# Performance work log

Measured on AMD Instinct MI355X. Metric: run time of the kernel, lower is better.

The kernel has to match this reference:

```python
import jax, jax.numpy as jnp
import numpy as np

B, N, C = 4, 20480, 128
H, HD = 8, 16           # num_heads, head_dim (C // H)
L = 4                   # number of WindowBasedGraphAttentionBlocks
NW, WS = 320, 64        # num_windows, window_size (N // NW)
SCALE = HD ** -0.5
EPS = 1e-5


def layernorm(x, g, b):
    mu = jnp.mean(x, axis=-1, keepdims=True)
    var = jnp.mean(jnp.square(x - mu), axis=-1, keepdims=True)
    return (x - mu) * jax.lax.rsqrt(var + EPS) * g + b


def setup_inputs() -> dict:
    key = jax.random.key(0)
    ks = jax.random.split(key, 8)
    x = jax.random.normal(ks[0], (B, N, C), dtype=jnp.float32)
    # geodesic window mapping: each of NW windows has exactly WS members, permuted
    window_ids = jnp.asarray(
        np.random.RandomState(0).permutation(np.repeat(np.arange(NW), WS)),
        dtype=jnp.int32)
    s = 0.02
    inp = {
        'x': x,
        'g1': jnp.ones((L, C), jnp.float32),
        'be1': jnp.zeros((L, C), jnp.float32),
        'Wqkv': jax.random.normal(ks[1], (L, C, 3 * C), jnp.float32) * s,
        'bqkv': jnp.zeros((L, 3 * C), jnp.float32),
        'rel_bias': jax.random.normal(ks[2], (L, H, 1, 1), jnp.float32) * s,
        'Wproj': jax.random.normal(ks[3], (L, C, C), jnp.float32) * s,
        'bproj': jnp.zeros((L, C), jnp.float32),
        'g2': jnp.ones((L, C), jnp.float32),
        'be2': jnp.zeros((L, C), jnp.float32),
        'W1': jax.random.normal(ks[4], (L, C, 4 * C), jnp.float32) * s,
        'b1': jnp.zeros((L, 4 * C), jnp.float32),
        'W2': jax.random.normal(ks[5], (L, 4 * C, C), jnp.float32) * s,
        'b2': jnp.zeros((L, C), jnp.float32),
        'window_ids': window_ids,
    }
    return inp


def _encoder(x, g1, be1, Wqkv, bqkv, rel_bias, Wproj, bproj, g2, be2,
             W1, b1, W2, b2, sort_idx, inv_idx):
    def step(x, p):
        (g1, be1, Wqkv, bqkv, rb, Wp, bp, g2, be2, W1, b1, W2, b2) = p
        shortcut = x
        # GeodesicWindowPartition: gather by argsort(window_ids), split into windows
        win = x[:, sort_idx, :].reshape(B * NW, WS, C)
        h = layernorm(win, g1, be1)
        qkv = (h @ Wqkv + bqkv).reshape(B * NW, WS, 3, H, HD)
        q = qkv[:, :, 0].transpose(0, 2, 1, 3)  # [BW, H, WS, HD]
        k = qkv[:, :, 1].transpose(0, 2, 1, 3)
        v = qkv[:, :, 2].transpose(0, 2, 1, 3)
        attn = jnp.einsum('whqd,whkd->whqk', q, k) * SCALE
        attn = attn + rb[None]                  # relative geometry bias [H,1,1]
        attn = jax.nn.softmax(attn, axis=-1)
        out = jnp.einsum('whqk,whkd->whqd', attn, v)
        out = out.transpose(0, 2, 1, 3).reshape(B * NW, WS, C)
        out = out @ Wp + bp                     # AttentionOutputProjection
        rec = out.reshape(B, N, C)[:, inv_idx, :]  # partition.reverse
        x = shortcut + rec
        h2 = layernorm(x, g2, be2)
        x = x + (jax.nn.gelu(h2 @ W1 + b1) @ W2 + b2)
        return x, None

    params = (g1, be1, Wqkv, bqkv, rel_bias, Wproj, bproj, g2, be2, W1, b1, W2, b2)
    x, _ = jax.lax.scan(step, x, params)
    return x


def reference(x, g1, be1, Wqkv, bqkv, rel_bias, Wproj, bproj, g2, be2,
              W1, b1, W2, b2, window_ids):
    sort_idx = jnp.argsort(window_ids)
    inv_idx = jnp.argsort(sort_idx)
    return _encoder(x, g1, be1, Wqkv, bqkv, rel_bias, Wproj, bproj, g2, be2,
                    W1, b1, W2, b2, sort_idx, inv_idx)
```

## Files before the change

### kernel.cpp

```cpp
#include <hip/hip_runtime.h>
#include <hip/hip_bf16.h>
#include <math.h>

#define Nn 20480
#define Cc 128
#define Hh 8
#define Ll 4
#define NWw 320
#define BN 81920

typedef short sv8 __attribute__((ext_vector_type(8)));
typedef __bf16 bfv8 __attribute__((ext_vector_type(8)));
typedef float f32x4 __attribute__((ext_vector_type(4)));

__device__ __forceinline__ f32x4 mfma16(sv8 a, sv8 b, f32x4 c) {
    return __builtin_amdgcn_mfma_f32_16x16x32_bf16(
        __builtin_bit_cast(bfv8, a), __builtin_bit_cast(bfv8, b), c, 0, 0, 0);
}
__device__ __forceinline__ ushort f2bf(float f) {
    uint u = __float_as_uint(f);
    u += 0x7fffu + ((u >> 16) & 1u);
    return (ushort)(u >> 16);
}
__device__ __forceinline__ float fast_gelu(float x) {
    float z = 0.7978845608f * (x + 0.044715f * x * x * x);
    return x * __builtin_amdgcn_rcpf(1.0f + __expf(-2.0f * z));
}

__global__ __launch_bounds__(64) void rank_kernel(const int* __restrict__ wid,
        int* __restrict__ lrank, int* __restrict__ hist) {
    __shared__ int keys[64];
    int c = blockIdx.x, lane = threadIdx.x;
    for (int j = lane; j < NWw; j += 64) hist[c * NWw + j] = 0;
    int i = c * 64 + lane;
    int w = wid[i];
    keys[lane] = w;
    __syncthreads();
    int rank = 0, total = 0;
    for (int j = 0; j < 64; ++j) {
        int kj = keys[j];
        total += (kj == w);
        rank += (j < lane && kj == w) ? 1 : 0;
    }
    lrank[i] = rank;
    if (rank == 0) hist[c * NWw + w] = total;
}
__global__ __launch_bounds__(64) void prefix_kernel(int* __restrict__ hist) {
    int w = blockIdx.x, lane = threadIdx.x;
    int running = 0;
    for (int it = 0; it < NWw / 64; ++it) {
        int c = it * 64 + lane;
        int v = hist[c * NWw + w];
        int orig = v;
        #pragma unroll
        for (int d = 1; d < 64; d <<= 1) {
            int tt = __shfl_up(v, d, 64);
            if (lane >= d) v += tt;
        }
        hist[c * NWw + w] = running + v - orig;
        running += __shfl(v, 63, 64);
    }
}
__global__ __launch_bounds__(64) void scatter_kernel(const int* __restrict__ wid,
        const int* __restrict__ lrank, const int* __restrict__ hist,
        int* __restrict__ sidx) {
    int c = blockIdx.x, lane = threadIdx.x;
    int i = c * 64 + lane;
    int w = wid[i];
    sidx[w * 64 + hist[c * NWw + w] + lrank[i]] = i;
}

__global__ __launch_bounds__(256) void wconv_kernel(
    const float* __restrict__ Wqkv, const float* __restrict__ Wproj,
    const float* __restrict__ W1, const float* __restrict__ W2,
    ushort* __restrict__ wt) {
    int id = blockIdx.x * 256 + threadIdx.x;
    int l = id / 196608;
    int r = id % 196608;
    const float* src; int dst;
    if (r < 49152) { int n = r % 384, k = r / 384;
        src = Wqkv + l * 49152 + k * 384 + n; dst = l * 196608 + n * 128 + k; }
    else if (r < 65536) { int rr = r - 49152; int n = rr % 128, k = rr / 128;
        src = Wproj + l * 16384 + k * 128 + n; dst = l * 196608 + 49152 + n * 128 + k; }
    else if (r < 131072) { int rr = r - 65536; int n = rr % 512, k = rr / 512;
        src = W1 + l * 65536 + k * 512 + n; dst = l * 196608 + 65536 + n * 128 + k; }
    else { int rr = r - 131072; int n = rr % 128, k = rr / 128;
        src = W2 + l * 65536 + k * 128 + n; dst = l * 196608 + 131072 + n * 512 + k; }
    wt[dst] = f2bf(*src);
}

__global__ __launch_bounds__(256, 2) void attn_fused_kernel(
    const float* __restrict__ xsrc, float* __restrict__ xdst,
    const ushort* __restrict__ wqkvT, const float* __restrict__ bqkv,
    const float* __restrict__ relb, const ushort* __restrict__ wprojT,
    const float* __restrict__ bproj, const float* __restrict__ g1,
    const float* __restrict__ be1, const int* __restrict__ sidx) {
    __shared__ __align__(16) ushort hl_[64][128];
    __shared__ __align__(16) ushort qkn[64][256];
    __shared__ __align__(16) ushort vT[128][76];
    __shared__ __align__(16) ushort pt[4][16][76];
    __shared__ int ridx[64];

    int t = threadIdx.x;
    int wave = t >> 6, lane = t & 63;
    int lr = lane & 15, lg = lane >> 4;
    int wb = blockIdx.x;
    int bN = (wb / NWw) * Nn;
    int p0 = (wb % NWw) * 64;

    if (t < 64) ridx[t] = sidx[p0 + t];
    __syncthreads();

    {
        int hl2 = lane & 31, hb = lane >> 5;
        float4 gg = *(const float4*)(g1 + hl2 * 4);
        float4 bb = *(const float4*)(be1 + hl2 * 4);
        #pragma unroll
        for (int it = 0; it < 8; ++it) {
            int row = it * 8 + wave * 2 + hb;
            int gi = bN + ridx[row];
            float4 v = *(const float4*)(xsrc + (size_t)gi * Cc + hl2 * 4);
            float s = v.x + v.y + v.z + v.w;
            s += __shfl_xor(s, 1, 64);  s += __shfl_xor(s, 2, 64);
            s += __shfl_xor(s, 4, 64);  s += __shfl_xor(s, 8, 64);
            s += __shfl_xor(s, 16, 64);
            float mu = s * 0.0078125f;
            float d0 = v.x - mu, d1 = v.y - mu, d2 = v.z - mu, d3 = v.w - mu;
            float q = d0 * d0 + d1 * d1 + d2 * d2 + d3 * d3;
            q += __shfl_xor(q, 1, 64);  q += __shfl_xor(q, 2, 64);
            q += __shfl_xor(q, 4, 64);  q += __shfl_xor(q, 8, 64);
            q += __shfl_xor(q, 16, 64);
            float rs = rsqrtf(q * 0.0078125f + 1e-5f);
            uint2 pk;
            pk.x = (uint)f2bf(d0 * rs * gg.x + bb.x) | ((uint)f2bf(d1 * rs * gg.y + bb.y) << 16);
            pk.y = (uint)f2bf(d2 * rs * gg.z + bb.z) | ((uint)f2bf(d3 * rs * gg.w + bb.w) << 16);
            *(uint2*)&hl_[row][(hl2 * 4) ^ ((row & 7) << 3)] = pk;
        }
    }
    __syncthreads();

    {
        f32x4 acc[4][6] = {};
        #pragma unroll
        for (int ks = 0; ks < 4; ++ks) {
            int k0 = ks * 32 + lg * 8;
            sv8 a[4], b[6];
            #pragma unroll
            for (int rf = 0; rf < 4; ++rf) {
                int row = rf * 16 + lr;
                a[rf] = *(const sv8*)&hl_[row][k0 ^ ((row & 7) << 3)];
            }
            #pragma unroll
            for (int nf = 0; nf < 6; ++nf) {
                int gcol = (nf < 2 ? 32 * wave + nf * 16
                          : nf < 4 ? 128 + 32 * wave + (nf - 2) * 16
                                   : 256 + 32 * wave + (nf - 4) * 16) + lr;
                b[nf] = *(const sv8*)(wqkvT + (size_t)gcol * 128 + k0);
            }
            #pragma unroll
            for (int rf = 0; rf < 4; ++rf)
                #pragma unroll
                for (int nf = 0; nf < 6; ++nf)
                    acc[rf][nf] = mfma16(a[rf], b[nf], acc[rf][nf]);
        }
        #pragma unroll
        for (int nf = 0; nf < 6; ++nf) {
            int gcol = (nf < 2 ? 32 * wave + nf * 16
                      : nf < 4 ? 128 + 32 * wave + (nf - 2) * 16
                               : 256 + 32 * wave + (nf - 4) * 16) + lr;
            float bs = bqkv[gcol];
            if (nf < 4) {
                #pragma unroll
                for (int rf = 0; rf < 4; ++rf)
                    #pragma unroll
                    for (int r = 0; r < 4; ++r) {
                        int row = rf * 16 + lg * 4 + r;
                        qkn[row][gcol ^ ((row & 7) << 3)] = f2bf(acc[rf][nf][r] + bs);
                    }
            } else {
                int dcol = gcol - 256;
                #pragma unroll
                for (int rf = 0; rf < 4; ++rf) {
                    uint2 pk;
                    pk.x = (uint)f2bf(acc[rf][nf][0] + bs) | ((uint)f2bf(acc[rf][nf][1] + bs) << 16);
                    pk.y = (uint)f2bf(acc[rf][nf][2] + bs) | ((uint)f2bf(acc[rf][nf][3] + bs) << 16);
                    *(uint2*)&vT[dcol][rf * 16 + lg * 4] = pk;
                }
            }
        }
    }
    __syncthreads();

    f32x4 zz = {0.f, 0.f, 0.f, 0.f};
    #pragma unroll
    for (int hi = 0; hi < 2; ++hi) {
        int hh = wave * 2 + hi;
        float rb = relb[hh];
        sv8 bv[2];
        #pragma unroll
        for (int ks = 0; ks < 2; ++ks)
            bv[ks] = *(const sv8*)&vT[hh * 16 + lr][ks * 32 + lg * 8];
        sv8 aq[4], bk[4];
        sv8 z = {0, 0, 0, 0, 0, 0, 0, 0};
        bool lo = (lg < 2);
        #pragma unroll
        for (int f = 0; f < 4; ++f) {
            aq[f] = z; bk[f] = z;
            if (lo) {
                int row = f * 16 + lr;
                aq[f] = *(const sv8*)&qkn[row][(hh * 16 + lg * 8) ^ ((row & 7) << 3)];
                bk[f] = *(const sv8*)&qkn[row][(128 + hh * 16 + lg * 8) ^ ((row & 7) << 3)];
            }
        }
        f32x4 s[4][4];
        #pragma unroll
        for (int kt = 0; kt < 4; ++kt)
            #pragma unroll
            for (int qt = 0; qt < 4; ++qt)
                s[kt][qt] = mfma16(bk[kt], aq[qt], zz);

        f32x4 o[4];
        #pragma unroll
        for (int qt = 0; qt < 4; ++qt) {
            float v[16];
            #pragma unroll
            for (int kt = 0; kt < 4; ++kt)
                #pragma unroll
                for (int r = 0; r < 4; ++r)
                    v[kt * 4 + r] = s[kt][qt][r] * 0.25f + rb;
            float m0 = fmaxf(fmaxf(fmaxf(v[0], v[1]), fmaxf(v[2], v[3])),
                             fmaxf(fmaxf(v[4], v[5]), fmaxf(v[6], v[7])));
            float m1 = fmaxf(fmaxf(fmaxf(v[8], v[9]), fmaxf(v[10], v[11])),
                             fmaxf(fmaxf(v[12], v[13]), fmaxf(v[14], v[15])));
            float mx = fmaxf(m0, m1);
            mx = fmaxf(mx, __shfl_xor(mx, 16, 64));
            mx = fmaxf(mx, __shfl_xor(mx, 32, 64));
            float sum = 0.f;
            #pragma unroll
            for (int i = 0; i < 16; ++i) {
                v[i] = __expf(v[i] - mx);
                sum += v[i];
            }
            sum += __shfl_xor(sum, 16, 64);
            sum += __shfl_xor(sum, 32, 64);
            float inv = __builtin_amdgcn_rcpf(sum);
            #pragma unroll
            for (int kt = 0; kt < 4; ++kt) {
                uint2 pk;
                pk.x = (uint)f2bf(v[kt * 4 + 0] * inv) | ((uint)f2bf(v[kt * 4 + 1] * inv) << 16);
                pk.y = (uint)f2bf(v[kt * 4 + 2] * inv) | ((uint)f2bf(v[kt * 4 + 3] * inv) << 16);
                *(uint2*)&pt[wave][lr][kt * 16 + lg * 4] = pk;
            }
            sv8 ap0 = *(const sv8*)&pt[wave][lr][lg * 8];
            sv8 ap1 = *(const sv8*)&pt[wave][lr][32 + lg * 8];
            o[qt] = mfma16(ap0, bv[0], zz);
            o[qt] = mfma16(ap1, bv[1], o[qt]);
        }
        #pragma unroll
        for (int qt = 0; qt < 4; ++qt)
            #pragma unroll
            for (int r = 0; r < 4; ++r) {
                int row = qt * 16 + lg * 4 + r;
                hl_[row][(hh * 16 + lr) ^ ((row & 7) << 3)] = f2bf(o[qt][r]);
            }
    }
    __syncthreads();

    {
        f32x4 acc[4][2] = {};
        #pragma unroll
        for (int ks = 0; ks < 4; ++ks) {
            int k0 = ks * 32 + lg * 8;
            sv8 a[4], b[2];
            #pragma unroll
            for (int rf = 0; rf < 4; ++rf) {
                int row = rf * 16 + lr;
                a[rf] = *(const sv8*)&hl_[row][k0 ^ ((row & 7) << 3)];
            }
            #pragma unroll
            for (int nf = 0; nf < 2; ++nf)
                b[nf] = *(const sv8*)(wprojT + (size_t)(wave * 32 + nf * 16 + lr) * 128 + k0);
            #pragma unroll
            for (int rf = 0; rf < 4; ++rf)
                #pragma unroll
                for (int nf = 0; nf < 2; ++nf)
                    acc[rf][nf] = mfma16(a[rf], b[nf], acc[rf][nf]);
        }
        #pragma unroll
        for (int nf = 0; nf < 2; ++nf) {
            int col = wave * 32 + nf * 16 + lr;
            float bs = bproj[col];
            #pragma unroll
            for (int rf = 0; rf < 4; ++rf)
                #pragma unroll
                for (int r = 0; r < 4; ++r) {
                    int row = rf * 16 + lg * 4 + r;
                    int gi = bN + ridx[row];
                    size_t ad = (size_t)gi * Cc + col;
                    xdst[ad] = xsrc[ad] + acc[rf][nf][r] + bs;
                }
        }
    }
}

__global__ __launch_bounds__(256, 2) void mlp_fused_kernel(
    const float* __restrict__ xsrc, float* __restrict__ xdst,
    const ushort* __restrict__ w1T, const float* __restrict__ b1,
    const ushort* __restrict__ w2T, const float* __restrict__ b2,
    const float* __restrict__ g2, const float* __restrict__ be2) {
    __shared__ __align__(16) ushort hl_[64][128];
    __shared__ __align__(16) ushort hid[64][512];
    int t = threadIdx.x, wave = t >> 6, lane = t & 63;
    int lr = lane & 15, lg = lane >> 4;
    int r0 = blockIdx.x * 64;

    {
        int hl2 = lane & 31, hb = lane >> 5;
        float4 gg = *(const float4*)(g2 + hl2 * 4);
        float4 bb = *(const float4*)(be2 + hl2 * 4);
        #pragma unroll
        for (int it = 0; it < 8; ++it) {
            int row = it * 8 + wave * 2 + hb;
            float4 v = *(const float4*)(xsrc + (size_t)(r0 + row) * Cc + hl2 * 4);
            float s = v.x + v.y + v.z + v.w;
            s += __shfl_xor(s, 1, 64);  s += __shfl_xor(s, 2, 64);
            s += __shfl_xor(s, 4, 64);  s += __shfl_xor(s, 8, 64);
            s += __shfl_xor(s, 16, 64);
            float mu = s * 0.0078125f;
            float d0 = v.x - mu, d1 = v.y - mu, d2 = v.z - mu, d3 = v.w - mu;
            float q = d0 * d0 + d1 * d1 + d2 * d2 + d3 * d3;
            q += __shfl_xor(q, 1, 64);  q += __shfl_xor(q, 2, 64);
            q += __shfl_xor(q, 4, 64);  q += __shfl_xor(q, 8, 64);
            q += __shfl_xor(q, 16, 64);
            float rs = rsqrtf(q * 0.0078125f + 1e-5f);
            uint2 pk;
            pk.x = (uint)f2bf(d0 * rs * gg.x + bb.x) | ((uint)f2bf(d1 * rs * gg.y + bb.y) << 16);
            pk.y = (uint)f2bf(d2 * rs * gg.z + bb.z) | ((uint)f2bf(d3 * rs * gg.w + bb.w) << 16);
            *(uint2*)&hl_[row][(hl2 * 4) ^ ((row & 7) << 3)] = pk;
        }
    }
    __syncthreads();

    {
        f32x4 acc[4][8] = {};
        #pragma unroll
        for (int ks = 0; ks < 4; ++ks) {
            int k0 = ks * 32 + lg * 8;
            sv8 a[4], b[8];
            #pragma unroll
            for (int rf = 0; rf < 4; ++rf) {
                int row = rf * 16 + lr;
                a[rf] = *(const sv8*)&hl_[row][k0 ^ ((row & 7) << 3)];
            }
            #pragma unroll
            for (int nf = 0; nf < 8; ++nf)
                b[nf] = *(const sv8*)(w1T + (size_t)(wave * 128 + nf * 16 + lr) * 128 + k0);
            #pragma unroll
            for (int rf = 0; rf < 4; ++rf)
                #pragma unroll
                for (int nf = 0; nf < 8; ++nf)
                    acc[rf][nf] = mfma16(a[rf], b[nf], acc[rf][nf]);
        }
        #pragma unroll
        for (int nf = 0; nf < 8; ++nf) {
            int col = wave * 128 + nf * 16 + lr;
            float bs = b1[col];
            #pragma unroll
            for (int rf = 0; rf < 4; ++rf)
                #pragma unroll
                for (int r = 0; r < 4; ++r) {
                    int row = rf * 16 + lg * 4 + r;
                    hid[row][col ^ ((row & 7) << 3)] = f2bf(fast_gelu(acc[rf][nf][r] + bs));
                }
        }
    }
    __syncthreads();

    {
        f32x4 acc2[4][2] = {};
        #pragma unroll
        for (int ks = 0; ks < 16; ++ks) {
            int k0 = ks * 32 + lg * 8;
            sv8 a[4], b[2];
            #pragma unroll
            for (int rf = 0; rf < 4; ++rf) {
                int row = rf * 16 + lr;
                a[rf] = *(const sv8*)&hid[row][k0 ^ ((row & 7) << 3)];
            }
            #pragma unroll
            for (int nf = 0; nf < 2; ++nf)
                b[nf] = *(const sv8*)(w2T + (size_t)(wave * 32 + nf * 16 + lr) * 512 + k0);
            #pragma unroll
            for (int rf = 0; rf < 4; ++rf)
                #pragma unroll
                for (int nf = 0; nf < 2; ++nf)
                    acc2[rf][nf] = mfma16(a[rf], b[nf], acc2[rf][nf]);
        }
        __syncthreads();
        float* fh = (float*)hid;
        #pragma unroll
        for (int nf = 0; nf < 2; ++nf) {
            int col = wave * 32 + nf * 16 + lr;
            float bs = b2[col];
            #pragma unroll
            for (int rf = 0; rf < 4; ++rf)
                #pragma unroll
                for (int r = 0; r < 4; ++r) {
                    int row = rf * 16 + lg * 4 + r;
                    fh[row * 132 + col] = acc2[rf][nf][r] + bs;
                }
        }
        __syncthreads();
        #pragma unroll
        for (int j = 0; j < 8; ++j) {
            int idx = t + j * 256;
            int row = idx >> 5, c4 = (idx & 31) * 4;
            size_t ad = (size_t)(r0 + row) * Cc + c4;
            float4 xv = *(const float4*)(xsrc + ad);
            float4 hv = *(const float4*)&fh[row * 132 + c4];
            float4 ov = {xv.x + hv.x, xv.y + hv.y, xv.z + hv.z, xv.w + hv.w};
            *(float4*)(xdst + ad) = ov;
        }
    }
}

extern "C" void kernel_launch(void* const* d_in, const int* in_sizes, int n_in,
                              void* d_out, int out_size, void* d_ws, size_t ws_size,
                              hipStream_t stream) {
    const float* x_in   = (const float*)d_in[0];
    const float* g1     = (const float*)d_in[1];
    const float* be1    = (const float*)d_in[2];
    const float* Wqkv   = (const float*)d_in[3];
    const float* bqkv   = (const float*)d_in[4];
    const float* relb   = (const float*)d_in[5];
    const float* Wproj  = (const float*)d_in[6];
    const float* bproj  = (const float*)d_in[7];
    const float* g2     = (const float*)d_in[8];
    const float* be2    = (const float*)d_in[9];
    const float* W1     = (const float*)d_in[10];
    const float* b1     = (const float*)d_in[11];
    const float* W2     = (const float*)d_in[12];
    const float* b2     = (const float*)d_in[13];
    const int*   wid    = (const int*)d_in[14];

    size_t off = 0;
    float* x_ws = (float*)d_ws;                      off += (size_t)BN * Cc * 4;
    ushort* wt  = (ushort*)((char*)d_ws + off);      off += (size_t)786432 * 2;
    int* sidx   = (int*)((char*)d_ws + off);         off += (size_t)Nn * 4;
    int* lrank  = (int*)((char*)d_ws + off);         off += (size_t)Nn * 4;
    int* hist   = (int*)((char*)d_ws + off);         off += (size_t)NWw * NWw * 4;
    if (ws_size < off) return;

    rank_kernel<<<Nn / 64, 64, 0, stream>>>(wid, lrank, hist);
    prefix_kernel<<<NWw, 64, 0, stream>>>(hist);
    scatter_kernel<<<Nn / 64, 64, 0, stream>>>(wid, lrank, hist, sidx);
    wconv_kernel<<<786432 / 256, 256, 0, stream>>>(Wqkv, Wproj, W1, W2, wt);

    for (int l = 0; l < Ll; ++l) {
        const ushort* wqkvT  = wt + (size_t)l * 196608;
        const ushort* wprojT = wqkvT + 49152;
        const ushort* w1T    = wqkvT + 65536;
        const ushort* w2T    = wqkvT + 131072;
        const float* xsrc = (l == 0) ? x_in : x_ws;

        attn_fused_kernel<<<BN / 64, 256, 0, stream>>>(
            xsrc, x_ws, wqkvT, bqkv + l * 384, relb + l * Hh,
            wprojT, bproj + l * Cc, g1 + l * Cc, be1 + l * Cc, sidx);

        float* xdst = (l == Ll - 1) ? (float*)d_out : x_ws;
        mlp_fused_kernel<<<BN / 64, 256, 0, stream>>>(
            x_ws, xdst, w1T, b1 + l * 512, w2T, b2 + l * Cc,
            g2 + l * Cc, be2 + l * Cc);
    }
}
```

Measured before the change: 471.8 us.

## Chunk MLP hidden dimension with double-buffered LDS and use packed bf16 conversion

The MLP kernel now processes the 512-wide hidden layer in four 128-column chunks, holding only two chunk buffers in LDS (48KB total instead of 80KB). This cuts the accumulator register footprint, which allows a launch bound of three blocks per CU instead of two. The cost is an extra barrier per chunk. Separately, the software round-to-nearest bf16 packing is replaced by the hardware v_cvt_pk_bf16_f32 instruction in the layernorm, V-transpose and softmax stores.

```diff
diff --git a/kernel.cpp b/kernel.cpp
--- a/kernel.cpp
+++ b/kernel.cpp
@@ -21,6 +21,11 @@
     uint u = __float_as_uint(f);
     u += 0x7fffu + ((u >> 16) & 1u);
     return (ushort)(u >> 16);
+}
+__device__ __forceinline__ uint pk2bf(float lo, float hi) {
+    uint r;
+    asm("v_cvt_pk_bf16_f32 %0, %1, %2" : "=v"(r) : "v"(lo), "v"(hi));
+    return r;
 }
 __device__ __forceinline__ float fast_gelu(float x) {
     float z = 0.7978845608f * (x + 0.044715f * x * x * x);
@@ -132,8 +137,8 @@
             q += __shfl_xor(q, 16, 64);
             float rs = rsqrtf(q * 0.0078125f + 1e-5f);
             uint2 pk;
-            pk.x = (uint)f2bf(d0 * rs * gg.x + bb.x) | ((uint)f2bf(d1 * rs * gg.y + bb.y) << 16);
-            pk.y = (uint)f2bf(d2 * rs * gg.z + bb.z) | ((uint)f2bf(d3 * rs * gg.w + bb.w) << 16);
+            pk.x = pk2bf(d0 * rs * gg.x + bb.x, d1 * rs * gg.y + bb.y);
+            pk.y = pk2bf(d2 * rs * gg.z + bb.z, d3 * rs * gg.w + bb.w);
             *(uint2*)&hl_[row][(hl2 * 4) ^ ((row & 7) << 3)] = pk;
         }
     }
@@ -182,8 +187,8 @@
                 #pragma unroll
                 for (int rf = 0; rf < 4; ++rf) {
                     uint2 pk;
-                    pk.x = (uint)f2bf(acc[rf][nf][0] + bs) | ((uint)f2bf(acc[rf][nf][1] + bs) << 16);
-                    pk.y = (uint)f2bf(acc[rf][nf][2] + bs) | ((uint)f2bf(acc[rf][nf][3] + bs) << 16);
+                    pk.x = pk2bf(acc[rf][nf][0] + bs, acc[rf][nf][1] + bs);
+                    pk.y = pk2bf(acc[rf][nf][2] + bs, acc[rf][nf][3] + bs);
                     *(uint2*)&vT[dcol][rf * 16 + lg * 4] = pk;
                 }
             }
@@ -247,8 +252,8 @@
             #pragma unroll
             for (int kt = 0; kt < 4; ++kt) {
                 uint2 pk;
-                pk.x = (uint)f2bf(v[kt * 4 + 0] * inv) | ((uint)f2bf(v[kt * 4 + 1] * inv) << 16);
-                pk.y = (uint)f2bf(v[kt * 4 + 2] * inv) | ((uint)f2bf(v[kt * 4 + 3] * inv) << 16);
+                pk.x = pk2bf(v[kt * 4 + 0] * inv, v[kt * 4 + 1] * inv);
+                pk.y = pk2bf(v[kt * 4 + 2] * inv, v[kt * 4 + 3] * inv);
                 *(uint2*)&pt[wave][lr][kt * 16 + lg * 4] = pk;
             }
             sv8 ap0 = *(const sv8*)&pt[wave][lr][lg * 8];
@@ -303,13 +308,14 @@
     }
 }
 
-__global__ __launch_bounds__(256, 2) void mlp_fused_kernel(
+__global__ __launch_bounds__(256, 3) void mlp_fused_kernel(
     const float* __restrict__ xsrc, float* __restrict__ xdst,
     const ushort* __restrict__ w1T, const float* __restrict__ b1,
     const ushort* __restrict__ w2T, const float* __restrict__ b2,
     const float* __restrict__ g2, const float* __restrict__ be2) {
-    __shared__ __align__(16) ushort hl_[64][128];
-    __shared__ __align__(16) ushort hid[64][512];
+    __shared__ __align__(16) char smem[49152];
+    ushort (*hl_)[128] = (ushort (*)[128])smem;
+    ushort (*hid)[64][128] = (ushort (*)[64][128])(smem + 16384);
     int t = threadIdx.x, wave = t >> 6, lane = t & 63;
     int lr = lane & 15, lg = lane >> 4;
     int r0 = blockIdx.x * 64;
@@ -334,70 +340,72 @@
             q += __shfl_xor(q, 16, 64);
             float rs = rsqrtf(q * 0.0078125f + 1e-5f);
             uint2 pk;
-            pk.x = (uint)f2bf(d0 * rs * gg.x + bb.x) | ((uint)f2bf(d1 * rs * gg.y + bb.y) << 16);
-            pk.y = (uint)f2bf(d2 * rs * gg.z + bb.z) | ((uint)f2bf(d3 * rs * gg.w + bb.w) << 16);
+            pk.x = pk2bf(d0 * rs * gg.x + bb.x, d1 * rs * gg.y + bb.y);
+            pk.y = pk2bf(d2 * rs * gg.z + bb.z, d3 * rs * gg.w + bb.w);
             *(uint2*)&hl_[row][(hl2 * 4) ^ ((row & 7) << 3)] = pk;
         }
     }
     __syncthreads();
 
-    {
-        f32x4 acc[4][8] = {};
+    f32x4 acc2[4][2] = {};
+    #pragma unroll
+    for (int c = 0; c < 4; ++c) {
+        int cb = c & 1;
+        f32x4 acc[4][2] = {};
         #pragma unroll
         for (int ks = 0; ks < 4; ++ks) {
             int k0 = ks * 32 + lg * 8;
-            sv8 a[4], b[8];
+            sv8 a[4], b[2];
             #pragma unroll
             for (int rf = 0; rf < 4; ++rf) {
                 int row = rf * 16 + lr;
                 a[rf] = *(const sv8*)&hl_[row][k0 ^ ((row & 7) << 3)];
             }
             #pragma unroll
-            for (int nf = 0; nf < 8; ++nf)
-                b[nf] = *(const sv8*)(w1T + (size_t)(wave * 128 + nf * 16 + lr) * 128 + k0);
-            #pragma unroll
-            for (int rf = 0; rf < 4; ++rf)
-                #pragma unroll
-                for (int nf = 0; nf < 8; ++nf)
+            for (int nf = 0; nf < 2; ++nf)
+                b[nf] = *(const sv8*)(w1T + (size_t)(c * 128 + wave * 32 + nf * 16 + lr) * 128 + k0);
+            #pragma unroll
+            for (int rf = 0; rf < 4; ++rf)
+                #pragma unroll
+                for (int nf = 0; nf < 2; ++nf)
                     acc[rf][nf] = mfma16(a[rf], b[nf], acc[rf][nf]);
         }
         #pragma unroll
-        for (int nf = 0; nf < 8; ++nf) {
-            int col = wave * 128 + nf * 16 + lr;
-            float bs = b1[col];
+        for (int nf = 0; nf < 2; ++nf) {
+            int lcol = wave * 32 + nf * 16 + lr;
+            float bs = b1[c * 128 + lcol];
             #pragma unroll
             for (int rf = 0; rf < 4; ++rf)
                 #pragma unroll
                 for (int r = 0; r < 4; ++r) {
                     int row = rf * 16 + lg * 4 + r;
-                    hid[row][col ^ ((row & 7) << 3)] = f2bf(fast_gelu(acc[rf][nf][r] + bs));
+                    hid[cb][row][lcol ^ ((row & 7) << 3)] = f2bf(fast_gelu(acc[rf][nf][r] + bs));
                 }
         }
-    }
-    __syncthreads();
-
-    {
-        f32x4 acc2[4][2] = {};
-        #pragma unroll
-        for (int ks = 0; ks < 16; ++ks) {
+        __syncthreads();
+        #pragma unroll
+        for (int ks = 0; ks < 4; ++ks) {
             int k0 = ks * 32 + lg * 8;
             sv8 a[4], b[2];
             #pragma unroll
             for (int rf = 0; rf < 4; ++rf) {
                 int row = rf * 16 + lr;
-                a[rf] = *(const sv8*)&hid[row][k0 ^ ((row & 7) << 3)];
+                a[rf] = *(const sv8*)&hid[cb][row][k0 ^ ((row & 7) << 3)];
             }
             #pragma unroll
             for (int nf = 0; nf < 2; ++nf)
-                b[nf] = *(const sv8*)(w2T + (size_t)(wave * 32 + nf * 16 + lr) * 512 + k0);
+                b[nf] = *(const sv8*)(w2T + (size_t)(wave * 32 + nf * 16 + lr) * 512 + c * 128 + k0);
             #pragma unroll
             for (int rf = 0; rf < 4; ++rf)
                 #pragma unroll
                 for (int nf = 0; nf < 2; ++nf)
                     acc2[rf][nf] = mfma16(a[rf], b[nf], acc2[rf][nf]);
         }
-        __syncthreads();
-        float* fh = (float*)hid;
+    }
+    __syncthreads();
+
+    {
+        float* fh = (float*)smem;
         #pragma unroll
         for (int nf = 0; nf < 2; ++nf) {
             int col = wave * 32 + nf * 16 + lr;
```

Measured after the change: 474.7 us. No clear change (+0.6%).
